# Kernel tuning notes

Hardware: AMD Instinct MI355X
Metric: run time of the kernel (lower is better)

## Reference

```python
import jax, jax.numpy as jnp
import numpy as np

N_SRC = 100000
N_DST = 20000
E = 640000
IN_FEATS = 256
NUM_HEADS = 4
OUT_FEATS = 32
NEG_SLOPE = 0.2


def setup_inputs() -> dict:
    key = jax.random.key(0)
    ks = jax.random.split(key, 8)
    x = jax.random.normal(ks[0], (N_SRC, IN_FEATS), dtype=jnp.float32)
    src_idx = jax.random.randint(ks[1], (E,), 0, N_SRC)
    dst_idx = jax.random.randint(ks[2], (E,), 0, N_DST)
    dst_to_src = jax.random.randint(ks[3], (N_DST,), 0, N_SRC)
    # parameters (xavier-ish scale)
    W = jax.random.normal(ks[4], (IN_FEATS, NUM_HEADS * OUT_FEATS), dtype=jnp.float32) * (1.0 / np.sqrt(IN_FEATS))
    attn_l = jax.random.normal(ks[5], (NUM_HEADS, OUT_FEATS), dtype=jnp.float32) * 0.1
    attn_r = jax.random.normal(ks[6], (NUM_HEADS, OUT_FEATS), dtype=jnp.float32) * 0.1
    return {"x": x, "W": W, "attn_l": attn_l, "attn_r": attn_r,
            "src_idx": src_idx, "dst_idx": dst_idx, "dst_to_src": dst_to_src}


def reference(x, W, attn_l, attn_r, src_idx, dst_idx, dst_to_src):
    # fc + reshape to heads: [N_src, H, D]
    h = (x @ W).reshape(N_SRC, NUM_HEADS, OUT_FEATS)
    # per-src-node left attention score: [N_src, H]
    el = jnp.einsum('nhd,hd->nh', h, attn_l)
    # self_gather: dst nodes are a subset of src nodes
    h_dst = h[dst_to_src]                       # [N_dst, H, D]
    er = jnp.einsum('nhd,hd->nh', h_dst, attn_r)  # [N_dst, H]
    # apply_edge + leaky_relu: per-edge scores [E, H]
    e = el[src_idx] + er[dst_idx]
    e = jnp.where(e >= 0, e, NEG_SLOPE * e)
    # NOTE: original code normalizes leaky_relu(e) directly (no exp)
    sum_e = jax.ops.segment_sum(e, dst_idx, num_segments=N_DST)  # [N_dst, H]
    attention = e / sum_e[dst_idx]              # [E, H]
    # attention_gather: weighted scatter-add of src features to dst
    msg = attention[:, :, None] * h[src_idx]    # [E, H, D]
    out = jax.ops.segment_sum(msg, dst_idx, num_segments=N_DST)  # [N_dst, H, D]
    return out
```

## Files before the change

### kernel.cpp

```cpp
#include <hip/hip_runtime.h>

#define N_SRC 100000
#define N_DST 20000
#define NE 640000
#define IN_F 256
#define NH 4
#define DF 32
#define NCOL 128

__global__ void k_prep(const float* __restrict__ W,
                       const float* __restrict__ attn_l,
                       const float* __restrict__ attn_r,
                       double* __restrict__ Wlr_t) {
    int k = threadIdx.x;
    for (int j = 0; j < 8; ++j) {
        const float* attn = (j < 4) ? attn_l : attn_r;
        int hh = j & 3;
        double s = 0.0;
        for (int d = 0; d < DF; ++d)
            s += (double)W[k * NCOL + hh * DF + d] * (double)attn[hh * DF + d];
        Wlr_t[(size_t)j * IN_F + k] = s;
    }
}

__global__ __launch_bounds__(256) void k_gemm(const float* __restrict__ x,
                                              const float* __restrict__ W,
                                              const double* __restrict__ Wlr_t,
                                              const int* __restrict__ dst_idx,
                                              float* __restrict__ h,
                                              double* __restrict__ el,
                                              int* __restrict__ cnt) {
    __shared__ float xs[32][68];
    __shared__ double wlds[4][66];
    const int tid = threadIdx.x;
    const int row0 = blockIdx.x * 32;
    const int c0 = (tid & 31) * 4;
    const int r0 = (tid >> 5) * 4;
    const int srow = tid >> 3;
    const int shh = tid & 3;
    const int shalf = (tid >> 2) & 1;

    const int sr0 = tid >> 4,          sq0 = (tid & 15) * 4;
    const int sr1 = (256 + tid) >> 4,  sq1 = (tid & 15) * 4;
    const int wj = tid >> 6, wk = tid & 63;

    float acc[4][4];
#pragma unroll
    for (int j = 0; j < 4; ++j)
#pragma unroll
        for (int m = 0; m < 4; ++m) acc[j][m] = 0.f;
    double sacc = 0.0;

    float4 pf0 = *((const float4*)(x + (size_t)(row0 + sr0) * IN_F + sq0));
    float4 pf1 = *((const float4*)(x + (size_t)(row0 + sr1) * IN_F + sq1));
    double pfw = Wlr_t[(size_t)wj * IN_F + wk];

    for (int chunk = 0; chunk < 4; ++chunk) {
        const int kbase = chunk * 64;
        if (chunk) __syncthreads();
        *((float4*)&xs[sr0][sq0]) = pf0;
        *((float4*)&xs[sr1][sq1]) = pf1;
        wlds[wj][wk] = pfw;
        __syncthreads();

        if (chunk < 3) {
            const int nk = kbase + 64;
            pf0 = *((const float4*)(x + (size_t)(row0 + sr0) * IN_F + nk + sq0));
            pf1 = *((const float4*)(x + (size_t)(row0 + sr1) * IN_F + nk + sq1));
            pfw = Wlr_t[(size_t)wj * IN_F + nk + wk];
        }

#pragma unroll 4
        for (int kq = 0; kq < 64; kq += 4) {
            const float* wp = W + (size_t)(kbase + kq) * NCOL + c0;
            float4 w0 = *((const float4*)(wp));
            float4 w1 = *((const float4*)(wp + NCOL));
            float4 w2 = *((const float4*)(wp + 2 * NCOL));
            float4 w3 = *((const float4*)(wp + 3 * NCOL));
#pragma unroll
            for (int j = 0; j < 4; ++j) {
                float4 xv = *((const float4*)&xs[r0 + j][kq]);
                acc[j][0] += xv.x * w0.x + xv.y * w1.x + xv.z * w2.x + xv.w * w3.x;
                acc[j][1] += xv.x * w0.y + xv.y * w1.y + xv.z * w2.y + xv.w * w3.y;
                acc[j][2] += xv.x * w0.z + xv.y * w1.z + xv.z * w2.z + xv.w * w3.z;
                acc[j][3] += xv.x * w0.w + xv.y * w1.w + xv.z * w2.w + xv.w * w3.w;
            }
        }

        {
            const int kb = shalf * 32;
#pragma unroll 4
            for (int k = 0; k < 32; k += 4) {
                float4 xv = *((const float4*)&xs[srow][kb + k]);
                double2 wa = *((const double2*)&wlds[shh][kb + k]);
                double2 wb = *((const double2*)&wlds[shh][kb + k + 2]);
                sacc += (double)xv.x * wa.x + (double)xv.y * wa.y
                      + (double)xv.z * wb.x + (double)xv.w * wb.y;
            }
        }
    }

#pragma unroll
    for (int j = 0; j < 4; ++j) {
        int row = row0 + r0 + j;
        *((float4*)(h + (size_t)row * NCOL + c0)) =
            make_float4(acc[j][0], acc[j][1], acc[j][2], acc[j][3]);
    }

    sacc += __shfl_xor(sacc, 4);
    if (shalf == 0)
        el[(size_t)(row0 + srow) * NH + shh] = sacc;

    for (int e = blockIdx.x * 256 + tid; e < NE; e += gridDim.x * 256)
        atomicAdd(cnt + dst_idx[e], 1);
}

__global__ __launch_bounds__(1024) void k_scan(const int* __restrict__ cnt,
                                               int* __restrict__ offsets,
                                               int* __restrict__ cursor) {
    __shared__ int wsum[16];
    __shared__ int carry;
    int tid = threadIdx.x, lane = tid & 63, w = tid >> 6;
    if (tid == 0) carry = 0;
    __syncthreads();
    for (int base = 0; base < N_DST; base += 1024) {
        int i = base + tid;
        int v = (i < N_DST) ? cnt[i] : 0;
        int s = v;
#pragma unroll
        for (int off = 1; off < 64; off <<= 1) {
            int t = __shfl_up(s, off);
            if (lane >= off) s += t;
        }
        if (lane == 63) wsum[w] = s;
        __syncthreads();
        int wprefix = 0;
        for (int k = 0; k < w; ++k) wprefix += wsum[k];
        int incl = s + wprefix + carry;
        if (i < N_DST) {
            offsets[i + 1] = incl;
            cursor[i] = 0;
        }
        __syncthreads();
        if (tid == 1023) carry = incl;
        __syncthreads();
    }
    if (tid == 0) offsets[0] = 0;
}

__global__ __launch_bounds__(256) void k_fill(const int* __restrict__ src_idx,
                                              const int* __restrict__ dst_idx,
                                              const int* __restrict__ offsets,
                                              int* __restrict__ cursor,
                                              int* __restrict__ edge_src) {
    int gid = blockIdx.x * 256 + threadIdx.x;
    if (gid >= NE) return;
    int d = dst_idx[gid];
    int pos = offsets[d] + atomicAdd(cursor + d, 1);
    edge_src[pos] = src_idx[gid];
}

__global__ __launch_bounds__(256) void k_fused(const int* __restrict__ offsets,
                                               const int* __restrict__ edge_src,
                                               const double* __restrict__ el,
                                               const float* __restrict__ x,
                                               const double* __restrict__ Wlr_t,
                                               const int* __restrict__ dst_to_src,
                                               const float* __restrict__ h,
                                               float* __restrict__ out) {
    __shared__ double att_sh[4][4][68];
    __shared__ int    s_sh[4][64];

    const int w = threadIdx.x >> 6;
    const int lane = threadIdx.x & 63;
    const int d = blockIdx.x * 4 + w;
    if (d >= N_DST) return;
    const int beg = offsets[d];
    const int deg = offsets[d + 1] - beg;

    double er4[NH];
    {
        const int srcrow = dst_to_src[d];
        float4 xv = *((const float4*)(x + (size_t)srcrow * IN_F + lane * 4));
        const double xd[4] = {(double)xv.x, (double)xv.y, (double)xv.z, (double)xv.w};
#pragma unroll
        for (int hh = 0; hh < 4; ++hh) {
            const double* wp = Wlr_t + (size_t)(4 + hh) * IN_F + lane * 4;
            er4[hh] = xd[0] * wp[0] + xd[1] * wp[1] + xd[2] * wp[2] + xd[3] * wp[3];
        }
#pragma unroll
        for (int hh = 0; hh < 4; ++hh) {
#pragma unroll
            for (int m = 32; m >= 1; m >>= 1)
                er4[hh] += __shfl_xor(er4[hh], m);
        }
    }
    const double er0 = er4[0], er1 = er4[1], er2 = er4[2], er3 = er4[3];

    double sum0 = 0.0, sum1 = 0.0, sum2 = 0.0, sum3 = 0.0;
    double e0r = 0.0, e1r = 0.0, e2r = 0.0, e3r = 0.0;
    int s_first = 0;
    for (int j = lane; j < deg; j += 64) {
        int s = edge_src[beg + j];
        double2 ela = *((const double2*)(el + (size_t)s * NH));
        double2 elb = *((const double2*)(el + (size_t)s * NH + 2));
        double e0 = ela.x + er0; e0 = (e0 >= 0.0) ? e0 : 0.2 * e0;
        double e1 = ela.y + er1; e1 = (e1 >= 0.0) ? e1 : 0.2 * e1;
        double e2 = elb.x + er2; e2 = (e2 >= 0.0) ? e2 : 0.2 * e2;
        double e3 = elb.y + er3; e3 = (e3 >= 0.0) ? e3 : 0.2 * e3;
        sum0 += e0; sum1 += e1; sum2 += e2; sum3 += e3;
        if (j == lane) { s_first = s; e0r = e0; e1r = e1; e2r = e2; e3r = e3; }
    }
#pragma unroll
    for (int m = 32; m >= 1; m >>= 1) {
        sum0 += __shfl_xor(sum0, m);
        sum1 += __shfl_xor(sum1, m);
        sum2 += __shfl_xor(sum2, m);
        sum3 += __shfl_xor(sum3, m);
    }

    if (lane < deg) {
        s_sh[w][lane] = s_first;
        att_sh[w][0][lane] = e0r / sum0;
        att_sh[w][1][lane] = e1r / sum1;
        att_sh[w][2][lane] = e2r / sum2;
        att_sh[w][3][lane] = e3r / sum3;
    }

    const int js = lane >> 5;
    const int cq = lane & 31;
    const int hd = cq >> 3;
    const double Shd = (hd == 0) ? sum0 : (hd == 1) ? sum1 : (hd == 2) ? sum2 : sum3;
    const double erhd = (hd == 0) ? er0 : (hd == 1) ? er1 : (hd == 2) ? er2 : er3;

    double acc0 = 0.0, acc1 = 0.0, acc2 = 0.0, acc3 = 0.0;
    for (int j = js; j < deg; j += 2) {
        int s; double att;
        if (j < 64) {
            s = s_sh[w][j];
            att = att_sh[w][hd][j];
        } else {
            s = edge_src[beg + j];
            double e = el[(size_t)s * NH + hd] + erhd;
            e = (e >= 0.0) ? e : 0.2 * e;
            att = e / Shd;
        }
        float4 hv = *((const float4*)(h + (size_t)s * NCOL + cq * 4));
        acc0 += att * (double)hv.x;
        acc1 += att * (double)hv.y;
        acc2 += att * (double)hv.z;
        acc3 += att * (double)hv.w;
    }
    acc0 += __shfl_xor(acc0, 32);
    acc1 += __shfl_xor(acc1, 32);
    acc2 += __shfl_xor(acc2, 32);
    acc3 += __shfl_xor(acc3, 32);

    if (lane < 32) {
        *((float4*)(out + (size_t)d * NCOL + lane * 4)) =
            make_float4((float)acc0, (float)acc1, (float)acc2, (float)acc3);
    }
}

extern "C" void kernel_launch(void* const* d_in, const int* in_sizes, int n_in,
                              void* d_out, int out_size, void* d_ws, size_t ws_size,
                              hipStream_t stream) {
    const float* x      = (const float*)d_in[0];
    const float* W      = (const float*)d_in[1];
    const float* attn_l = (const float*)d_in[2];
    const float* attn_r = (const float*)d_in[3];
    const int* src_idx  = (const int*)d_in[4];
    const int* dst_idx  = (const int*)d_in[5];
    const int* dst_to_src = (const int*)d_in[6];
    float* out = (float*)d_out;

    char* p = (char*)d_ws;
    double* Wlr_t  = (double*)p;  p += (size_t)8 * IN_F * sizeof(double);
    double* el     = (double*)p;  p += (size_t)N_SRC * NH * sizeof(double);
    float*  h      = (float*)p;   p += (size_t)N_SRC * NCOL * sizeof(float);
    int*    cnt      = (int*)p;   p += (size_t)N_DST * sizeof(int);
    int*    offsets  = (int*)p;   p += (size_t)(N_DST + 1) * sizeof(int);
    int*    cursor   = (int*)p;   p += (size_t)N_DST * sizeof(int);
    int*    edge_src = (int*)p;   p += (size_t)NE * sizeof(int);

    hipMemsetAsync(cnt, 0, (size_t)N_DST * sizeof(int), stream);

    k_prep<<<1, 256, 0, stream>>>(W, attn_l, attn_r, Wlr_t);
    k_gemm<<<N_SRC / 32, 256, 0, stream>>>(x, W, Wlr_t, dst_idx, h, el, cnt);
    k_scan<<<1, 1024, 0, stream>>>(cnt, offsets, cursor);
    k_fill<<<(NE + 255) / 256, 256, 0, stream>>>(src_idx, dst_idx, offsets, cursor, edge_src);
    k_fused<<<N_DST / 4, 256, 0, stream>>>(offsets, edge_src, el, x, Wlr_t, dst_to_src, h, out);
}
```

Measured before the change: 275.5 us.

## Retile GEMM to 64-row blocks with wave-uniform 16-column W slices

The projection GEMM now uses 512-thread blocks covering 64 rows, with each thread owning one row and 16 columns. The column group is wave-uniform (readfirstlane), so W loads become scalar/broadcast loads instead of per-lane vector loads. The register prefetch of the next x chunk is dropped in favour of direct load-then-sync, and bounds checks are added for the partial last block. This trades software pipelining for less W traffic per FMA and higher arithmetic intensity per block, at the risk of exposed global-load latency and higher register pressure from 64 W values per iteration.

```diff
diff --git a/kernel.cpp b/kernel.cpp
--- a/kernel.cpp
+++ b/kernel.cpp
@@ -23,68 +23,84 @@
     }
 }
 
-__global__ __launch_bounds__(256) void k_gemm(const float* __restrict__ x,
+__global__ __launch_bounds__(512) void k_gemm(const float* __restrict__ x,
                                               const float* __restrict__ W,
                                               const double* __restrict__ Wlr_t,
                                               const int* __restrict__ dst_idx,
                                               float* __restrict__ h,
                                               double* __restrict__ el,
                                               int* __restrict__ cnt) {
-    __shared__ float xs[32][68];
+    __shared__ float xs[64][68];
     __shared__ double wlds[4][66];
     const int tid = threadIdx.x;
-    const int row0 = blockIdx.x * 32;
-    const int c0 = (tid & 31) * 4;
-    const int r0 = (tid >> 5) * 4;
+    const int row0 = blockIdx.x * 64;
+    const int lane = tid & 63;
+    const int cg = __builtin_amdgcn_readfirstlane(tid >> 6);
+    const int c0 = cg * 16;
     const int srow = tid >> 3;
     const int shh = tid & 3;
     const int shalf = (tid >> 2) & 1;
 
-    const int sr0 = tid >> 4,          sq0 = (tid & 15) * 4;
-    const int sr1 = (256 + tid) >> 4,  sq1 = (tid & 15) * 4;
-    const int wj = tid >> 6, wk = tid & 63;
-
-    float acc[4][4];
-#pragma unroll
-    for (int j = 0; j < 4; ++j)
-#pragma unroll
-        for (int m = 0; m < 4; ++m) acc[j][m] = 0.f;
+    float4 acc0 = make_float4(0.f, 0.f, 0.f, 0.f);
+    float4 acc1 = make_float4(0.f, 0.f, 0.f, 0.f);
+    float4 acc2 = make_float4(0.f, 0.f, 0.f, 0.f);
+    float4 acc3 = make_float4(0.f, 0.f, 0.f, 0.f);
     double sacc = 0.0;
-
-    float4 pf0 = *((const float4*)(x + (size_t)(row0 + sr0) * IN_F + sq0));
-    float4 pf1 = *((const float4*)(x + (size_t)(row0 + sr1) * IN_F + sq1));
-    double pfw = Wlr_t[(size_t)wj * IN_F + wk];
 
     for (int chunk = 0; chunk < 4; ++chunk) {
         const int kbase = chunk * 64;
         if (chunk) __syncthreads();
-        *((float4*)&xs[sr0][sq0]) = pf0;
-        *((float4*)&xs[sr1][sq1]) = pf1;
-        wlds[wj][wk] = pfw;
+#pragma unroll
+        for (int t = 0; t < 2; ++t) {
+            int i = t * 512 + tid;
+            int r = i >> 4;
+            int q = i & 15;
+            int row = row0 + r;
+            float4 v = make_float4(0.f, 0.f, 0.f, 0.f);
+            if (row < N_SRC)
+                v = *((const float4*)(x + (size_t)row * IN_F + kbase + q * 4));
+            *((float4*)&xs[r][q * 4]) = v;
+        }
+        if (tid < 256)
+            wlds[tid >> 6][tid & 63] = Wlr_t[(size_t)(tid >> 6) * IN_F + kbase + (tid & 63)];
         __syncthreads();
 
-        if (chunk < 3) {
-            const int nk = kbase + 64;
-            pf0 = *((const float4*)(x + (size_t)(row0 + sr0) * IN_F + nk + sq0));
-            pf1 = *((const float4*)(x + (size_t)(row0 + sr1) * IN_F + nk + sq1));
-            pfw = Wlr_t[(size_t)wj * IN_F + nk + wk];
-        }
-
-#pragma unroll 4
+#pragma unroll 1
         for (int kq = 0; kq < 64; kq += 4) {
             const float* wp = W + (size_t)(kbase + kq) * NCOL + c0;
-            float4 w0 = *((const float4*)(wp));
-            float4 w1 = *((const float4*)(wp + NCOL));
-            float4 w2 = *((const float4*)(wp + 2 * NCOL));
-            float4 w3 = *((const float4*)(wp + 3 * NCOL));
-#pragma unroll
-            for (int j = 0; j < 4; ++j) {
-                float4 xv = *((const float4*)&xs[r0 + j][kq]);
-                acc[j][0] += xv.x * w0.x + xv.y * w1.x + xv.z * w2.x + xv.w * w3.x;
-                acc[j][1] += xv.x * w0.y + xv.y * w1.y + xv.z * w2.y + xv.w * w3.y;
-                acc[j][2] += xv.x * w0.z + xv.y * w1.z + xv.z * w2.z + xv.w * w3.z;
-                acc[j][3] += xv.x * w0.w + xv.y * w1.w + xv.z * w2.w + xv.w * w3.w;
-            }
+            float4 r0a = *((const float4*)(wp + 0));
+            float4 r0b = *((const float4*)(wp + 4));
+            float4 r0c = *((const float4*)(wp + 8));
+            float4 r0d = *((const float4*)(wp + 12));
+            float4 r1a = *((const float4*)(wp + NCOL + 0));
+            float4 r1b = *((const float4*)(wp + NCOL + 4));
+            float4 r1c = *((const float4*)(wp + NCOL + 8));
+            float4 r1d = *((const float4*)(wp + NCOL + 12));
+            float4 r2a = *((const float4*)(wp + 2 * NCOL + 0));
+            float4 r2b = *((const float4*)(wp + 2 * NCOL + 4));
+            float4 r2c = *((const float4*)(wp + 2 * NCOL + 8));
+            float4 r2d = *((const float4*)(wp + 2 * NCOL + 12));
+            float4 r3a = *((const float4*)(wp + 3 * NCOL + 0));
+            float4 r3b = *((const float4*)(wp + 3 * NCOL + 4));
+            float4 r3c = *((const float4*)(wp + 3 * NCOL + 8));
+            float4 r3d = *((const float4*)(wp + 3 * NCOL + 12));
+            float4 xv = *((const float4*)&xs[lane][kq]);
+            acc0.x += xv.x * r0a.x + xv.y * r1a.x + xv.z * r2a.x + xv.w * r3a.x;
+            acc0.y += xv.x * r0a.y + xv.y * r1a.y + xv.z * r2a.y + xv.w * r3a.y;
+            acc0.z += xv.x * r0a.z + xv.y * r1a.z + xv.z * r2a.z + xv.w * r3a.z;
+            acc0.w += xv.x * r0a.w + xv.y * r1a.w + xv.z * r2a.w + xv.w * r3a.w;
+            acc1.x += xv.x * r0b.x + xv.y * r1b.x + xv.z * r2b.x + xv.w * r3b.x;
+            acc1.y += xv.x * r0b.y + xv.y * r1b.y + xv.z * r2b.y + xv.w * r3b.y;
+            acc1.z += xv.x * r0b.z + xv.y * r1b.z + xv.z * r2b.z + xv.w * r3b.z;
+            acc1.w += xv.x * r0b.w + xv.y * r1b.w + xv.z * r2b.w + xv.w * r3b.w;
+            acc2.x += xv.x * r0c.x + xv.y * r1c.x + xv.z * r2c.x + xv.w * r3c.x;
+            acc2.y += xv.x * r0c.y + xv.y * r1c.y + xv.z * r2c.y + xv.w * r3c.y;
+            acc2.z += xv.x * r0c.z + xv.y * r1c.z + xv.z * r2c.z + xv.w * r3c.z;
+            acc2.w += xv.x * r0c.w + xv.y * r1c.w + xv.z * r2c.w + xv.w * r3c.w;
+            acc3.x += xv.x * r0d.x + xv.y * r1d.x + xv.z * r2d.x + xv.w * r3d.x;
+            acc3.y += xv.x * r0d.y + xv.y * r1d.y + xv.z * r2d.y + xv.w * r3d.y;
+            acc3.z += xv.x * r0d.z + xv.y * r1d.z + xv.z * r2d.z + xv.w * r3d.z;
+            acc3.w += xv.x * r0d.w + xv.y * r1d.w + xv.z * r2d.w + xv.w * r3d.w;
         }
 
         {
@@ -100,18 +116,25 @@
         }
     }
 
-#pragma unroll
-    for (int j = 0; j < 4; ++j) {
-        int row = row0 + r0 + j;
-        *((float4*)(h + (size_t)row * NCOL + c0)) =
-            make_float4(acc[j][0], acc[j][1], acc[j][2], acc[j][3]);
+    {
+        int row = row0 + lane;
+        if (row < N_SRC) {
+            float* hp = h + (size_t)row * NCOL + c0;
+            *((float4*)(hp + 0)) = acc0;
+            *((float4*)(hp + 4)) = acc1;
+            *((float4*)(hp + 8)) = acc2;
+            *((float4*)(hp + 12)) = acc3;
+        }
     }
 
     sacc += __shfl_xor(sacc, 4);
-    if (shalf == 0)
-        el[(size_t)(row0 + srow) * NH + shh] = sacc;
-
-    for (int e = blockIdx.x * 256 + tid; e < NE; e += gridDim.x * 256)
+    {
+        int row = row0 + srow;
+        if (shalf == 0 && row < N_SRC)
+            el[(size_t)row * NH + shh] = sacc;
+    }
+
+    for (int e = blockIdx.x * 512 + tid; e < NE; e += gridDim.x * 512)
         atomicAdd(cnt + dst_idx[e], 1);
 }
 
@@ -286,7 +309,7 @@
     hipMemsetAsync(cnt, 0, (size_t)N_DST * sizeof(int), stream);
 
     k_prep<<<1, 256, 0, stream>>>(W, attn_l, attn_r, Wlr_t);
-    k_gemm<<<N_SRC / 32, 256, 0, stream>>>(x, W, Wlr_t, dst_idx, h, el, cnt);
+    k_gemm<<<(N_SRC + 63) / 64, 512, 0, stream>>>(x, W, Wlr_t, dst_idx, h, el, cnt);
     k_scan<<<1, 1024, 0, stream>>>(cnt, offsets, cursor);
     k_fill<<<(NE + 255) / 256, 256, 0, stream>>>(src_idx, dst_idx, offsets, cursor, edge_src);
     k_fused<<<N_DST / 4, 256, 0, stream>>>(offsets, edge_src, el, x, Wlr_t, dst_to_src, h, out);
```

Measured after the change: 263.7 us. -4.3%, faster.
